# Kernel optimization log

Measured on AMD Instinct MI355X. Metric: run time of the kernel, lower is better.

Reference implementation:

```python
import jax, jax.numpy as jnp
import numpy as np

B, I, H = 4096, 2048, 2048

def setup_inputs() -> dict:
    key = jax.random.key(0)
    ks = jax.random.split(key, 7)
    sk = (1.0 / H) ** 0.5
    return {
        "x": jax.random.normal(ks[0], (B, I), dtype=jnp.float32),
        "prev_state": jax.random.normal(ks[1], (B, H), dtype=jnp.float32),
        "c_state": jax.random.normal(ks[2], (B, H), dtype=jnp.float32),
        "W_fg": jax.random.uniform(ks[3], (H, H + I), jnp.float32, -sk, sk),
        "W_ig": jax.random.uniform(ks[4], (H, H + I), jnp.float32, -sk, sk),
        "W_og": jax.random.uniform(ks[5], (H, H + I), jnp.float32, -sk, sk),
        "W_ol": jax.random.uniform(ks[6], (H, H + I), jnp.float32, -sk, sk),
    }

def reference(x, prev_state, c_state, W_fg, W_ig, W_og, W_ol):
    # concat_hx: [B, H+I]
    concat_hx = jnp.concatenate([prev_state, x], axis=1)
    # Fuse the 4 gate GEMMs into one [B, H+I] x [H+I, 4H] matmul
    W_all = jnp.concatenate([W_fg, W_ig, W_og, W_ol], axis=0)  # [4H, H+I]
    gates = concat_hx @ W_all.T  # [B, 4H]
    ft, it, ct_t, ot = jnp.split(jax.nn.sigmoid(gates), 4, axis=1)
    # NOTE: original uses sigmoid (not tanh) for the candidate cell state ct_t
    ct = ft * c_state + it * ct_t
    ht = ot * jnp.tanh(ct)
    return ht
```

## Files before the change

### kernel.cpp

```cpp
#include <hip/hip_runtime.h>
#include <hip/hip_bf16.h>
#include <cstdint>
#include <cstddef>


typedef __bf16 nbf16;
typedef nbf16 bf16x8 __attribute__((ext_vector_type(8)));
typedef float f32x4 __attribute__((ext_vector_type(4)));

static constexpr int MDIM = 4096;
static constexpr int NDIM = 8192;
static constexpr int KDIM = 4096;
static constexpr int HDIM = 2048;
static constexpr int KB   = KDIM * 2;

#define VMW10 asm volatile("s_waitcnt vmcnt(10)" ::: "memory")
#define VMW0  asm volatile("s_waitcnt vmcnt(0)" ::: "memory")
#define LGKM0 asm volatile("s_waitcnt lgkmcnt(0)" ::: "memory")
#define BAR   __builtin_amdgcn_s_barrier()
#define SB0   __builtin_amdgcn_sched_barrier(0)
#define PRIO1 __builtin_amdgcn_s_setprio(1)
#define PRIO0 __builtin_amdgcn_s_setprio(0)

__device__ __forceinline__ void async16(void* lds, const void* g) {
    __builtin_amdgcn_global_load_lds(
        (const __attribute__((address_space(1))) void*)g,
        (__attribute__((address_space(3))) void*)lds,
        16, 0, 0);
}

__device__ __forceinline__ float sigmoidf_(float x) {
    return 1.0f / (1.0f + __expf(-x));
}

__device__ __forceinline__ void stage_A(const char* Ab, int X, int t, char* slot,
                                        int wave, int r0, int cb) {
    const char* s = Ab + (size_t)(X * 64 + r0) * KB + t * 128 + cb;
    async16(slot + wave * 1024, s);
    async16(slot + (wave + 8) * 1024, s + (size_t)128 * KB);
}
__device__ __forceinline__ void stage_B(const char* Wb, int Y, int t, char* slot,
                                        int wave, int rB0, int cb) {
    const char* s = Wb + (size_t)(rB0 + Y * 32) * KB + t * 128 + cb;
    async16(slot + wave * 1024, s);
    async16(slot + (wave + 8) * 1024, s + (size_t)128 * KB);
}

__device__ __forceinline__ void read_A(bf16x8 (&d)[4][2], const char* hb,
                                       int ar, int kc0, int kc1) {
#pragma unroll
    for (int m = 0; m < 4; ++m) {
        d[m][0] = *(const bf16x8*)(hb + ar + m * 2048 + kc0);
        d[m][1] = *(const bf16x8*)(hb + ar + m * 2048 + kc1);
    }
}
__device__ __forceinline__ void read_B(bf16x8 (&d)[2][2], const char* hb,
                                       int br, int kc0, int kc1) {
#pragma unroll
    for (int j = 0; j < 2; ++j) {
        d[j][0] = *(const bf16x8*)(hb + br + j * 2048 + kc0);
        d[j][1] = *(const bf16x8*)(hb + br + j * 2048 + kc1);
    }
}
__device__ __forceinline__ void mfma16(f32x4 (&acc)[8][4], int mh, int Y,
                                       const bf16x8 (&a)[4][2],
                                       const bf16x8 (&b)[2][2]) {
#pragma unroll
    for (int m = 0; m < 4; ++m)
#pragma unroll
        for (int j = 0; j < 2; ++j) {
            acc[mh * 4 + m][Y * 2 + j] = __builtin_amdgcn_mfma_f32_16x16x32_bf16(
                a[m][0], b[j][0], acc[mh * 4 + m][Y * 2 + j], 0, 0, 0);
            acc[mh * 4 + m][Y * 2 + j] = __builtin_amdgcn_mfma_f32_16x16x32_bf16(
                a[m][1], b[j][1], acc[mh * 4 + m][Y * 2 + j], 0, 0, 0);
        }
}

__global__ __launch_bounds__(256) void k_concat_cast(
        const float* __restrict__ prev, const float* __restrict__ x,
        __hip_bfloat16* __restrict__ A) {
    const size_t total8 = (size_t)MDIM * KDIM / 8;
    const size_t stride = (size_t)gridDim.x * blockDim.x;
    for (size_t i = (size_t)blockIdx.x * blockDim.x + threadIdx.x; i < total8;
         i += stride) {
        size_t e = i * 8;
        size_t b = e >> 12;
        int k = (int)(e & (KDIM - 1));
        const float* src = (k < HDIM) ? (prev + b * HDIM + k)
                                      : (x + b * HDIM + (k - HDIM));
        float4 v0 = *(const float4*)src;
        float4 v1 = *(const float4*)(src + 4);
        union { __hip_bfloat16 h[8]; int4 q; } u;
        u.h[0] = __float2bfloat16(v0.x); u.h[1] = __float2bfloat16(v0.y);
        u.h[2] = __float2bfloat16(v0.z); u.h[3] = __float2bfloat16(v0.w);
        u.h[4] = __float2bfloat16(v1.x); u.h[5] = __float2bfloat16(v1.y);
        u.h[6] = __float2bfloat16(v1.z); u.h[7] = __float2bfloat16(v1.w);
        *(int4*)(A + e) = u.q;
    }
}

__global__ __launch_bounds__(256) void k_cast_w(
        const float* __restrict__ w0, const float* __restrict__ w1,
        const float* __restrict__ w2, const float* __restrict__ w3,
        __hip_bfloat16* __restrict__ W) {
    const size_t per = (size_t)HDIM * KDIM;
    const size_t total8 = 4 * per / 8;
    const size_t stride = (size_t)gridDim.x * blockDim.x;
    for (size_t i = (size_t)blockIdx.x * blockDim.x + threadIdx.x; i < total8;
         i += stride) {
        size_t e = i * 8;
        int g = (int)(e >> 23);
        size_t rem = e & (per - 1);
        const float* src = (g == 0 ? w0 : g == 1 ? w1 : g == 2 ? w2 : w3) + rem;
        float4 v0 = *(const float4*)src;
        float4 v1 = *(const float4*)(src + 4);
        union { __hip_bfloat16 h[8]; int4 q; } u;
        u.h[0] = __float2bfloat16(v0.x); u.h[1] = __float2bfloat16(v0.y);
        u.h[2] = __float2bfloat16(v0.z); u.h[3] = __float2bfloat16(v0.w);
        u.h[4] = __float2bfloat16(v1.x); u.h[5] = __float2bfloat16(v1.y);
        u.h[6] = __float2bfloat16(v1.z); u.h[7] = __float2bfloat16(v1.w);
        *(int4*)(W + e) = u.q;
    }
}

__global__ __launch_bounds__(512, 2) void k_gemm(
        const __hip_bfloat16* __restrict__ A, const __hip_bfloat16* __restrict__ W,
        __hip_bfloat16* __restrict__ G) {
    __shared__ __align__(16) char lds[131072];

    const int bid = blockIdx.x;
    const int swz = (bid & 7) * 64 + (bid >> 3);
    const int mt = swz >> 5, nt = swz & 31;
    const int brow = mt * 256, bcol = nt * 256;

    const int tid = threadIdx.x;
    const int wave = tid >> 6, lane = tid & 63;
    const int wr = wave >> 2, wc = wave & 3;

    const char* Ab = (const char*)A + (size_t)brow * KB;
    const char* Wb = (const char*)W + (size_t)bcol * KB;

    char* const Ah00 = lds;
    char* const Ah01 = lds + 16384;
    char* const Ah10 = lds + 32768;
    char* const Ah11 = lds + 49152;
    char* const Bh00 = lds + 65536;
    char* const Bh01 = lds + 81920;
    char* const Bh10 = lds + 98304;
    char* const Bh11 = lds + 114688;

    const int r0  = wave * 8 + (lane >> 3);
    const int rB0 = ((r0 >> 5) << 6) + (r0 & 31);
    const int cb  = (((lane & 7) ^ (lane >> 3)) << 4);
    const int kg  = lane >> 4;
    const int ar  = (wr * 64 + (lane & 15)) * 128;
    const int br  = (wc * 32 + (lane & 15)) * 128;
    const int kc0 = ((kg ^ (lane & 7)) << 4);
    const int kc1 = (((4 + kg) ^ (lane & 7)) << 4);

    f32x4 acc[8][4] = {};
    bf16x8 a0[4][2], a1[4][2], b0[2][2], b1[2][2];

    stage_B(Wb, 0, 0, Bh00, wave, rB0, cb);
    stage_A(Ab, 0, 0, Ah00, wave, r0, cb);
    stage_A(Ab, 1, 0, Ah01, wave, r0, cb);
    stage_B(Wb, 1, 0, Bh01, wave, rB0, cb);
    stage_B(Wb, 0, 1, Bh10, wave, rB0, cb);
    stage_A(Ab, 0, 1, Ah10, wave, r0, cb);
    stage_A(Ab, 1, 1, Ah11, wave, r0, cb);
    stage_B(Wb, 1, 1, Bh11, wave, rB0, cb);
    VMW10;
    SB0; BAR;
    read_A(a0, Ah00, ar, kc0, kc1);
    read_B(b0, Bh00, br, kc0, kc1);

    for (int i = 0; i < 32; ++i) {
        const int t2 = (2 * i + 2) & 63;
        const int t3 = (2 * i + 3) & 63;

        read_A(a1, Ah01, ar, kc0, kc1);
        stage_B(Wb, 0, t2, Bh00, wave, rB0, cb);
        VMW10; SB0; BAR; LGKM0; SB0;
        PRIO1; mfma16(acc, 0, 0, a0, b0); PRIO0;
        SB0; BAR;
        read_B(b1, Bh01, br, kc0, kc1);
        stage_A(Ab, 0, t2, Ah00, wave, r0, cb);
        VMW10; SB0; BAR; LGKM0; SB0;
        PRIO1; mfma16(acc, 1, 0, a1, b0); PRIO0;
        SB0; BAR;
        read_B(b0, Bh10, br, kc0, kc1);
        stage_A(Ab, 1, t2, Ah01, wave, r0, cb);
        VMW10; SB0; BAR; LGKM0; SB0;
        PRIO1; mfma16(acc, 1, 1, a1, b1); PRIO0;
        SB0; BAR;
        read_A(a1, Ah10, ar, kc0, kc1);
        stage_B(Wb, 1, t2, Bh01, wave, rB0, cb);
        VMW10; SB0; BAR; LGKM0; SB0;
        PRIO1; mfma16(acc, 0, 1, a0, b1); PRIO0;
        SB0; BAR;
        read_A(a0, Ah11, ar, kc0, kc1);
        stage_B(Wb, 0, t3, Bh10, wave, rB0, cb);
        VMW10; SB0; BAR; LGKM0; SB0;
        PRIO1; mfma16(acc, 0, 0, a1, b0); PRIO0;
        SB0; BAR;
        read_B(b1, Bh11, br, kc0, kc1);
        stage_A(Ab, 0, t3, Ah10, wave, r0, cb);
        VMW10; SB0; BAR; LGKM0; SB0;
        PRIO1; mfma16(acc, 1, 0, a0, b0); PRIO0;
        SB0; BAR;
        read_B(b0, Bh00, br, kc0, kc1);
        stage_A(Ab, 1, t3, Ah11, wave, r0, cb);
        VMW10; SB0; BAR; LGKM0; SB0;
        PRIO1; mfma16(acc, 1, 1, a0, b1); PRIO0;
        SB0; BAR;
        read_A(a0, Ah00, ar, kc0, kc1);
        stage_B(Wb, 1, t3, Bh11, wave, rB0, cb);
        VMW10; SB0; BAR; LGKM0; SB0;
        PRIO1; mfma16(acc, 0, 1, a1, b1); PRIO0;
        SB0; BAR;
    }

    VMW0;
    BAR;
    __hip_bfloat16* cl = (__hip_bfloat16*)lds;
    {
        const int rb = wr * 128 + ((lane >> 4) << 2);
        const int cbase = wc * 64 + (lane & 15);
        #pragma unroll
        for (int mi = 0; mi < 8; ++mi)
            #pragma unroll
            for (int ni = 0; ni < 4; ++ni)
                #pragma unroll
                for (int q = 0; q < 4; ++q)
                    cl[(rb + mi * 16 + q) * 256 + (cbase + ni * 16)] =
                        __float2bfloat16(acc[mi][ni][q]);
    }
    BAR;
    #pragma unroll
    for (int j = 0; j < 16; ++j) {
        const int o = j * 8192 + tid * 16;
        const int r = o >> 9, cbyte = o & 511;
        *(int4*)((char*)G + ((size_t)(brow + r) * NDIM + bcol) * 2 + cbyte) =
            *(const int4*)(lds + o);
    }
}

__global__ __launch_bounds__(256) void k_cell(
        const __hip_bfloat16* __restrict__ G, const float* __restrict__ c,
        float* __restrict__ out) {
    const size_t total8 = (size_t)MDIM * HDIM / 8;
    const size_t stride = (size_t)gridDim.x * blockDim.x;
    for (size_t i = (size_t)blockIdx.x * blockDim.x + threadIdx.x; i < total8;
         i += stride) {
        size_t e = i * 8;
        size_t b = e >> 11;
        int h = (int)(e & (HDIM - 1));
        const __hip_bfloat16* gb = G + b * NDIM + h;
        int4 vf = *(const int4*)(gb);
        int4 vi = *(const int4*)(gb + HDIM);
        int4 vc = *(const int4*)(gb + 2 * HDIM);
        int4 vo = *(const int4*)(gb + 3 * HDIM);
        float4 cs0 = *(const float4*)(c + e);
        float4 cs1 = *(const float4*)(c + e + 4);
        const __hip_bfloat16* pf = (const __hip_bfloat16*)&vf;
        const __hip_bfloat16* pi = (const __hip_bfloat16*)&vi;
        const __hip_bfloat16* pc = (const __hip_bfloat16*)&vc;
        const __hip_bfloat16* po = (const __hip_bfloat16*)&vo;
        float cse[8] = {cs0.x, cs0.y, cs0.z, cs0.w, cs1.x, cs1.y, cs1.z, cs1.w};
        float r[8];
        #pragma unroll
        for (int k = 0; k < 8; ++k) {
            float ft = sigmoidf_(__bfloat162float(pf[k]));
            float it = sigmoidf_(__bfloat162float(pi[k]));
            float ctt = sigmoidf_(__bfloat162float(pc[k]));
            float ot = sigmoidf_(__bfloat162float(po[k]));
            float ct = ft * cse[k] + it * ctt;
            r[k] = ot * tanhf(ct);
        }
        float4 o0 = {r[0], r[1], r[2], r[3]};
        float4 o1 = {r[4], r[5], r[6], r[7]};
        *(float4*)(out + e) = o0;
        *(float4*)(out + e + 4) = o1;
    }
}

extern "C" void kernel_launch(void* const* d_in, const int* in_sizes, int n_in,
                              void* d_out, int out_size, void* d_ws, size_t ws_size,
                              hipStream_t stream) {
    const float* x    = (const float*)d_in[0];
    const float* prev = (const float*)d_in[1];
    const float* cst  = (const float*)d_in[2];
    const float* wfg  = (const float*)d_in[3];
    const float* wig  = (const float*)d_in[4];
    const float* wog  = (const float*)d_in[5];
    const float* wol  = (const float*)d_in[6];
    float* out = (float*)d_out;

    char* ws = (char*)d_ws;
    __hip_bfloat16* Abf   = (__hip_bfloat16*)(ws);
    __hip_bfloat16* Wbf   = (__hip_bfloat16*)(ws + 33554432);
    __hip_bfloat16* gates = (__hip_bfloat16*)(ws + 33554432 + 67108864);

    k_concat_cast<<<2048, 256, 0, stream>>>(prev, x, Abf);
    k_cast_w<<<2048, 256, 0, stream>>>(wfg, wig, wog, wol, Wbf);
    k_gemm<<<512, 512, 0, stream>>>(Abf, Wbf, gates);
    k_cell<<<2048, 256, 0, stream>>>(gates, cst, out);
}
```

Measured before the change: 309.7 us.

## Fuse LSTM cell epilogue into GEMM via interleaved gate weight layout

The weight cast now interleaves the four gate matrices row by row, so each GEMM output tile holds all four gates for 64 hidden units. The GEMM epilogue stages the tile through LDS in two halves and applies the sigmoid/tanh cell update directly, writing the final fp32 output. This removes the bf16 gates buffer round trip through global memory and the separate cell kernel launch. The block-to-tile mapping is also changed to group tiles per XCD, and the epilogue gains an extra barrier and more arithmetic while running at the GEMM's occupancy.

```diff
diff --git a/kernel.cpp b/kernel.cpp
--- a/kernel.cpp
+++ b/kernel.cpp
@@ -103,15 +103,17 @@
         const float* __restrict__ w0, const float* __restrict__ w1,
         const float* __restrict__ w2, const float* __restrict__ w3,
         __hip_bfloat16* __restrict__ W) {
-    const size_t per = (size_t)HDIM * KDIM;
-    const size_t total8 = 4 * per / 8;
+    const size_t total8 = (size_t)NDIM * KDIM / 8;
     const size_t stride = (size_t)gridDim.x * blockDim.x;
     for (size_t i = (size_t)blockIdx.x * blockDim.x + threadIdx.x; i < total8;
          i += stride) {
         size_t e = i * 8;
-        int g = (int)(e >> 23);
-        size_t rem = e & (per - 1);
-        const float* src = (g == 0 ? w0 : g == 1 ? w1 : g == 2 ? w2 : w3) + rem;
+        int n = (int)(e >> 12);
+        int k = (int)(e & (KDIM - 1));
+        int g = n & 3;
+        size_t h = (size_t)(n >> 2);
+        const float* src = (g == 0 ? w0 : g == 1 ? w1 : g == 2 ? w2 : w3)
+                           + h * KDIM + k;
         float4 v0 = *(const float4*)src;
         float4 v1 = *(const float4*)(src + 4);
         union { __hip_bfloat16 h[8]; int4 q; } u;
@@ -125,12 +127,13 @@
 
 __global__ __launch_bounds__(512, 2) void k_gemm(
         const __hip_bfloat16* __restrict__ A, const __hip_bfloat16* __restrict__ W,
-        __hip_bfloat16* __restrict__ G) {
+        const float* __restrict__ c, float* __restrict__ out) {
     __shared__ __align__(16) char lds[131072];
 
     const int bid = blockIdx.x;
-    const int swz = (bid & 7) * 64 + (bid >> 3);
-    const int mt = swz >> 5, nt = swz & 31;
+    const int xcd = bid & 7, j = bid >> 3;
+    const int mt = (xcd >> 2) * 8 + (j >> 3);
+    const int nt = (xcd & 3) * 8 + (j & 7);
     const int brow = mt * 256, bcol = nt * 256;
 
     const int tid = threadIdx.x;
@@ -183,36 +186,43 @@
         VMW10; SB0; BAR; LGKM0; SB0;
         PRIO1; mfma16(acc, 0, 0, a0, b0); PRIO0;
         SB0; BAR;
+
         read_B(b1, Bh01, br, kc0, kc1);
         stage_A(Ab, 0, t2, Ah00, wave, r0, cb);
         VMW10; SB0; BAR; LGKM0; SB0;
         PRIO1; mfma16(acc, 1, 0, a1, b0); PRIO0;
         SB0; BAR;
+
         read_B(b0, Bh10, br, kc0, kc1);
         stage_A(Ab, 1, t2, Ah01, wave, r0, cb);
         VMW10; SB0; BAR; LGKM0; SB0;
         PRIO1; mfma16(acc, 1, 1, a1, b1); PRIO0;
         SB0; BAR;
+
         read_A(a1, Ah10, ar, kc0, kc1);
         stage_B(Wb, 1, t2, Bh01, wave, rB0, cb);
         VMW10; SB0; BAR; LGKM0; SB0;
         PRIO1; mfma16(acc, 0, 1, a0, b1); PRIO0;
         SB0; BAR;
+
         read_A(a0, Ah11, ar, kc0, kc1);
         stage_B(Wb, 0, t3, Bh10, wave, rB0, cb);
         VMW10; SB0; BAR; LGKM0; SB0;
         PRIO1; mfma16(acc, 0, 0, a1, b0); PRIO0;
         SB0; BAR;
+
         read_B(b1, Bh11, br, kc0, kc1);
         stage_A(Ab, 0, t3, Ah10, wave, r0, cb);
         VMW10; SB0; BAR; LGKM0; SB0;
         PRIO1; mfma16(acc, 1, 0, a0, b0); PRIO0;
         SB0; BAR;
+
         read_B(b0, Bh00, br, kc0, kc1);
         stage_A(Ab, 1, t3, Ah11, wave, r0, cb);
         VMW10; SB0; BAR; LGKM0; SB0;
         PRIO1; mfma16(acc, 1, 1, a0, b1); PRIO0;
         SB0; BAR;
+
         read_A(a0, Ah00, ar, kc0, kc1);
         stage_B(Wb, 1, t3, Bh11, wave, rB0, cb);
         VMW10; SB0; BAR; LGKM0; SB0;
@@ -223,64 +233,47 @@
     VMW0;
     BAR;
     __hip_bfloat16* cl = (__hip_bfloat16*)lds;
-    {
-        const int rb = wr * 128 + ((lane >> 4) << 2);
-        const int cbase = wc * 64 + (lane & 15);
+    const int h0 = bcol >> 2;
+    #pragma unroll
+    for (int p = 0; p < 2; ++p) {
+        if (p) BAR;
+        if (wr == p) {
+            const int rb = ((lane >> 4) << 2);
+            const int cbase = wc * 64 + (lane & 15);
+            #pragma unroll
+            for (int mi = 0; mi < 8; ++mi)
+                #pragma unroll
+                for (int ni = 0; ni < 4; ++ni)
+                    #pragma unroll
+                    for (int q = 0; q < 4; ++q)
+                        cl[(rb + mi * 16 + q) * 256 + (cbase + ni * 16)] =
+                            __float2bfloat16(acc[mi][ni][q]);
+        }
+        BAR;
         #pragma unroll
-        for (int mi = 0; mi < 8; ++mi)
+        for (int rnd = 0; rnd < 4; ++rnd) {
+            const int row = rnd * 32 + (tid >> 4);
+            const int ccol = (tid & 15) * 16;
+            union { int4 q[2]; __hip_bfloat16 h[16]; } v;
+            v.q[0] = *(const int4*)&cl[row * 256 + ccol];
+            v.q[1] = *(const int4*)&cl[row * 256 + ccol + 8];
+            const size_t R = (size_t)(brow + p * 128 + row);
+            const int hh = h0 + (tid & 15) * 4;
+            float4 cc = *(const float4*)(c + R * HDIM + hh);
+            float cs[4] = {cc.x, cc.y, cc.z, cc.w};
+            float ht[4];
             #pragma unroll
-            for (int ni = 0; ni < 4; ++ni)
-                #pragma unroll
-                for (int q = 0; q < 4; ++q)
-                    cl[(rb + mi * 16 + q) * 256 + (cbase + ni * 16)] =
-                        __float2bfloat16(acc[mi][ni][q]);
-    }
-    BAR;
-    #pragma unroll
-    for (int j = 0; j < 16; ++j) {
-        const int o = j * 8192 + tid * 16;
-        const int r = o >> 9, cbyte = o & 511;
-        *(int4*)((char*)G + ((size_t)(brow + r) * NDIM + bcol) * 2 + cbyte) =
-            *(const int4*)(lds + o);
-    }
-}
-
-__global__ __launch_bounds__(256) void k_cell(
-        const __hip_bfloat16* __restrict__ G, const float* __restrict__ c,
-        float* __restrict__ out) {
-    const size_t total8 = (size_t)MDIM * HDIM / 8;
-    const size_t stride = (size_t)gridDim.x * blockDim.x;
-    for (size_t i = (size_t)blockIdx.x * blockDim.x + threadIdx.x; i < total8;
-         i += stride) {
-        size_t e = i * 8;
-        size_t b = e >> 11;
-        int h = (int)(e & (HDIM - 1));
-        const __hip_bfloat16* gb = G + b * NDIM + h;
-        int4 vf = *(const int4*)(gb);
-        int4 vi = *(const int4*)(gb + HDIM);
-        int4 vc = *(const int4*)(gb + 2 * HDIM);
-        int4 vo = *(const int4*)(gb + 3 * HDIM);
-        float4 cs0 = *(const float4*)(c + e);
-        float4 cs1 = *(const float4*)(c + e + 4);
-        const __hip_bfloat16* pf = (const __hip_bfloat16*)&vf;
-        const __hip_bfloat16* pi = (const __hip_bfloat16*)&vi;
-        const __hip_bfloat16* pc = (const __hip_bfloat16*)&vc;
-        const __hip_bfloat16* po = (const __hip_bfloat16*)&vo;
-        float cse[8] = {cs0.x, cs0.y, cs0.z, cs0.w, cs1.x, cs1.y, cs1.z, cs1.w};
-        float r[8];
-        #pragma unroll
-        for (int k = 0; k < 8; ++k) {
-            float ft = sigmoidf_(__bfloat162float(pf[k]));
-            float it = sigmoidf_(__bfloat162float(pi[k]));
-            float ctt = sigmoidf_(__bfloat162float(pc[k]));
-            float ot = sigmoidf_(__bfloat162float(po[k]));
-            float ct = ft * cse[k] + it * ctt;
-            r[k] = ot * tanhf(ct);
+            for (int u = 0; u < 4; ++u) {
+                float ft  = sigmoidf_(__bfloat162float(v.h[4 * u + 0]));
+                float it  = sigmoidf_(__bfloat162float(v.h[4 * u + 1]));
+                float ctt = sigmoidf_(__bfloat162float(v.h[4 * u + 2]));
+                float ot  = sigmoidf_(__bfloat162float(v.h[4 * u + 3]));
+                float ct  = ft * cs[u] + it * ctt;
+                ht[u] = ot * tanhf(ct);
+            }
+            float4 o = {ht[0], ht[1], ht[2], ht[3]};
+            *(float4*)(out + R * HDIM + hh) = o;
         }
-        float4 o0 = {r[0], r[1], r[2], r[3]};
-        float4 o1 = {r[4], r[5], r[6], r[7]};
-        *(float4*)(out + e) = o0;
-        *(float4*)(out + e + 4) = o1;
     }
 }
 
@@ -297,12 +290,10 @@
     float* out = (float*)d_out;
 
     char* ws = (char*)d_ws;
-    __hip_bfloat16* Abf   = (__hip_bfloat16*)(ws);
-    __hip_bfloat16* Wbf   = (__hip_bfloat16*)(ws + 33554432);
-    __hip_bfloat16* gates = (__hip_bfloat16*)(ws + 33554432 + 67108864);
+    __hip_bfloat16* Abf = (__hip_bfloat16*)(ws);
+    __hip_bfloat16* Wbf = (__hip_bfloat16*)(ws + 33554432);
 
     k_concat_cast<<<2048, 256, 0, stream>>>(prev, x, Abf);
     k_cast_w<<<2048, 256, 0, stream>>>(wfg, wig, wog, wol, Wbf);
-    k_gemm<<<512, 512, 0, stream>>>(Abf, Wbf, gates);
-    k_cell<<<2048, 256, 0, stream>>>(gates, cst, out);
-}
+    k_gemm<<<512, 512, 0, stream>>>(Abf, Wbf, cst, out);
+}
```

Measured after the change: 287.0 us. -7.3%, faster.
